# Performance work log

Measured on AMD Instinct MI355X. Metric: run time of the kernel, lower is better.

Reference implementation:

```python
import jax, jax.numpy as jnp
import numpy as np

N = 512          # pedestrians in scene
T = 12           # decode steps
OBS = 8
FEAT = 2
LAT = 32
COND = 64
LSTM_IN = 128
HID = 64         # lstm_hidden_size == context_state_size
CTX = 64
EMB = 32         # Pooling_net spatial embedding dim
MLP_IN = EMB + 2 * CTX   # 160
MLP_MID = 64
BOT = CTX        # bottleneck_dim = h_dim
IN_DEC = COND + LAT + CTX + FEAT  # 162


def setup_inputs() -> dict:
    key = jax.random.key(0)
    ks = jax.random.split(key, 24)
    s = 0.1
    return {
        "last_position": jax.random.normal(ks[0], (N, FEAT), jnp.float32),
        "c": jax.random.normal(ks[1], (N, COND), jnp.float32),
        "z": jax.random.normal(ks[2], (N, LAT), jnp.float32),
        "obs_traj_pos": jax.random.normal(ks[3], (OBS, N, FEAT), jnp.float32),
        "nei_index": jax.random.randint(ks[4], (T, N, N), 0, 2, jnp.int32),
        "nei_num_index": jax.random.randint(ks[5], (N,), 0, N, jnp.int32),
        "h0": jax.random.normal(ks[6], (N, HID), jnp.float32),
        "c0": jax.random.normal(ks[7], (N, HID), jnp.float32),
        "eps": jax.random.normal(ks[8], (T, N, FEAT), jnp.float32),
        "W_in": jax.random.normal(ks[9], (IN_DEC, LSTM_IN), jnp.float32) * s,
        "b_in": jnp.zeros((LSTM_IN,), jnp.float32),
        "W_ih": jax.random.normal(ks[10], (4 * HID, LSTM_IN), jnp.float32) * s,
        "W_hh": jax.random.normal(ks[11], (4 * HID, HID), jnp.float32) * s,
        "b_ih": jnp.zeros((4 * HID,), jnp.float32),
        "b_hh": jnp.zeros((4 * HID,), jnp.float32),
        "W_l2p": jax.random.normal(ks[12], (HID // 2 + CTX, FEAT), jnp.float32) * s,
        "b_l2p": jnp.zeros((FEAT,), jnp.float32),
        "W_sp": jax.random.normal(ks[13], (FEAT, EMB), jnp.float32) * s,
        "b_sp": jnp.zeros((EMB,), jnp.float32),
        "W1": jax.random.normal(ks[14], (MLP_IN, MLP_MID), jnp.float32) * s,
        "b1": jnp.zeros((MLP_MID,), jnp.float32),
        "W2": jax.random.normal(ks[15], (MLP_MID, BOT), jnp.float32) * s,
        "b2": jnp.zeros((BOT,), jnp.float32),
    }


def reference(last_position, c, z, obs_traj_pos, nei_index, nei_num_index,
              h0, c0, eps, W_in, b_in, W_ih, W_hh, b_ih, b_hh,
              W_l2p, b_l2p, W_sp, b_sp, W1, b1, W2, b2):
    sg = jax.lax.stop_gradient
    half = HID // 2
    neg_inf = jnp.float32(-jnp.inf)

    def pooling(mask, lstm_state, pos):
        # mask: [N,N] bool; lstm_state: [N,CTX]; pos: [N,2]
        corr = pos[:, None, :] - pos[None, :, :]           # [N,N,2] pos[i]-pos[j]
        r = corr @ W_sp + b_sp                              # [N,N,EMB]
        hj = jnp.broadcast_to(lstm_state[None, :, :], (N, N, CTX))
        hi = jnp.broadcast_to(lstm_state[:, None, :], (N, N, CTX))
        x = jnp.concatenate([r, hj, hi], axis=-1)           # [N,N,160]
        h1 = jax.nn.relu(x @ W1 + b1)
        h2 = jax.nn.relu(h1 @ W2 + b2)                      # [N,N,BOT]
        Hm = jnp.where(mask[:, :, None], h2, neg_inf)       # scatter of valid rows
        pool = Hm.max(axis=1)                               # max over neighbors j
        return jnp.where(pool == neg_inf, 0.0, pool)

    def lstm_cell(x, h, cs):
        gates = x @ W_ih.T + b_ih + h @ W_hh.T + b_hh
        i, f, g, o = jnp.split(gates, 4, axis=-1)
        c_new = jax.nn.sigmoid(f) * cs + jax.nn.sigmoid(i) * jnp.tanh(g)
        h_new = jax.nn.sigmoid(o) * jnp.tanh(c_new)
        return h_new, c_new

    def step(carry, xs):
        prev_pos, h, cs, ctx, cur_abs = carry
        nei_t, eps_t = xs
        emb = jnp.concatenate([sg(prev_pos), sg(c), sg(z), sg(ctx)], axis=-1)
        x = jax.nn.relu(emb @ W_in + b_in)
        h, cs = lstm_cell(x, h, cs)
        ctx = pooling(nei_t > 0, h, cur_abs)
        mu = jnp.concatenate([h[:, :half], ctx], -1) @ W_l2p + b_l2p
        logvar = jnp.concatenate([h[:, half:], ctx], -1) @ W_l2p + b_l2p
        pos = mu + eps_t * jnp.exp(0.5 * logvar)
        cur_abs = sg(cur_abs + pos)
        return (pos, h, cs, ctx, cur_abs), (pos, mu, logvar)

    ctx0 = jnp.zeros((N, CTX), jnp.float32)
    carry0 = (last_position, h0, c0, ctx0, obs_traj_pos[-1])
    _, (pre_pos, mean, var) = jax.lax.scan(step, carry0, (nei_index, eps))
    return pre_pos, mean, var
```

## Files before the change

kernel.cpp:

```cpp
#include <hip/hip_runtime.h>
#include <math.h>

#define NP 512
#define TT 12

typedef float f32x4 __attribute__((ext_vector_type(4)));
typedef __bf16 bf16x8 __attribute__((ext_vector_type(8)));

#define OFF_CURABS 0
#define OFF_A      2048
#define OFF_B      67584
#define OFF_H      100352
#define OFF_CS     133120
#define OFF_WIHT   165888
#define OFF_WHHT   198656
#define OFF_WC     215040
#define OFF_BASE   215168

__global__ __launch_bounds__(256) void init_k(
    const float* __restrict__ obs, const float* __restrict__ W_ih,
    const float* __restrict__ W_hh, const float* __restrict__ W_sp,
    const float* __restrict__ b_sp, const float* __restrict__ W1,
    const float* __restrict__ b1, float* __restrict__ ws) {
  int tid = blockIdx.x * 256 + threadIdx.x;
  if (tid < 1024) ws[OFF_CURABS + tid] = obs[7 * 1024 + tid];
  if (tid < 32768) {
    int k = tid >> 8, g = tid & 255;
    ws[OFF_WIHT + tid] = W_ih[g * 128 + k];
  }
  if (tid < 16384) {
    int k = tid >> 8, g = tid & 255;
    ws[OFF_WHHT + tid] = W_hh[g * 64 + k];
  }
  if (tid < 128) {
    int d = tid >> 6, m = tid & 63;
    float s = 0.f;
    for (int e = 0; e < 32; ++e) s = fmaf(W_sp[d * 32 + e], W1[e * 64 + m], s);
    ws[OFF_WC + tid] = s;
  }
  if (tid < 64) {
    float s = b1[tid];
    for (int e = 0; e < 32; ++e) s = fmaf(b_sp[e], W1[e * 64 + tid], s);
    ws[OFF_BASE + tid] = s;
  }
}

__global__ __launch_bounds__(256) void step_k(
    const float* __restrict__ lastpos, const float* __restrict__ cc,
    const float* __restrict__ zz, const int* __restrict__ nei,
    const float* __restrict__ h0, const float* __restrict__ c0,
    const float* __restrict__ epsin,
    const float* __restrict__ W_in, const float* __restrict__ b_in,
    const float* __restrict__ b_ih, const float* __restrict__ b_hh,
    const float* __restrict__ Wl2p, const float* __restrict__ bl2p,
    const float* __restrict__ W1, const float* __restrict__ W2,
    const float* __restrict__ b2,
    float* __restrict__ out, float* __restrict__ ws, int s) {
  __shared__ __align__(16) __bf16 h1buf[4][32 * 72];
  __shared__ __align__(16) __bf16 W2T[64 * 72];
  __shared__ float absx[512], absy[512];
  __shared__ int   ml[512];
  __shared__ float wcl[128], bib[64], basev[64];
  __shared__ float red[4][64];
  __shared__ float hloc[64], csloc[64], ctxloc[64], prevp[2];
  __shared__ float emb[162], xpart[2][128], xvec[128], gl[256];

  int t = threadIdx.x;
  int b = blockIdx.x;
  int lane = t & 63, w = t >> 6;
  int quad = lane >> 4, col = lane & 15;

  if (t < 64) {
    if (s == 0) { hloc[t] = h0[b * 64 + t]; csloc[t] = c0[b * 64 + t]; ctxloc[t] = 0.f; }
    else        { hloc[t] = ws[OFF_H + b * 64 + t]; csloc[t] = ws[OFF_CS + b * 64 + t]; }
    basev[t] = ws[OFF_BASE + t];
  } else if (t < 192) {
    wcl[t - 64] = ws[OFF_WC + (t - 64)];
  } else if (s > 0) {
    bib[t - 192] = ws[OFF_B + b * 64 + (t - 192)];
  }
  if (s == 0 && t < 2) prevp[t] = lastpos[b * 2 + t];
  if (s > 0) {
    for (int e = t; e < 4096; e += 256)
      W2T[(e & 63) * 72 + (e >> 6)] = (__bf16)W2[e];
  }
  __syncthreads();

  if (s > 0) {
    int st = s - 1;
    bf16x8 bf00 = *(const bf16x8*)&W2T[(0 * 16 + col) * 72 + 0 * 32 + quad * 8];
    bf16x8 bf01 = *(const bf16x8*)&W2T[(0 * 16 + col) * 72 + 1 * 32 + quad * 8];
    bf16x8 bf10 = *(const bf16x8*)&W2T[(1 * 16 + col) * 72 + 0 * 32 + quad * 8];
    bf16x8 bf11 = *(const bf16x8*)&W2T[(1 * 16 + col) * 72 + 1 * 32 + quad * 8];
    bf16x8 bf20 = *(const bf16x8*)&W2T[(2 * 16 + col) * 72 + 0 * 32 + quad * 8];
    bf16x8 bf21 = *(const bf16x8*)&W2T[(2 * 16 + col) * 72 + 1 * 32 + quad * 8];
    bf16x8 bf30 = *(const bf16x8*)&W2T[(3 * 16 + col) * 72 + 0 * 32 + quad * 8];
    bf16x8 bf31 = *(const bf16x8*)&W2T[(3 * 16 + col) * 72 + 1 * 32 + quad * 8];
    float b2v0 = b2[col], b2v1 = b2[16 + col], b2v2 = b2[32 + col], b2v3 = b2[48 + col];

    int rb = st & 1, wbuf = rb ^ 1;
    const float* curabs  = ws + OFF_CURABS + rb * 1024;
    float*       curabsw = ws + OFF_CURABS + wbuf * 1024;
    const float* Aab = ws + OFF_A + rb * 32768;
    const int* neirow = nei + ((size_t)st * NP + b) * NP;
    {
      const float2* ca = (const float2*)curabs;
      for (int j = t; j < 512; j += 256) {
        float2 p = ca[j];
        absx[j] = p.x; absy[j] = p.y;
        ml[j] = neirow[j];
      }
    }
    __syncthreads();

    float px = absx[b], py = absy[b];
    float wcx = wcl[lane], wcy = wcl[64 + lane];
    float bi  = bib[lane];
    float vmax0 = 0.f, vmax1 = 0.f, vmax2 = 0.f, vmax3 = 0.f;
    __bf16* myh1 = h1buf[w];

    for (int c = 0; c < 4; ++c) {
      int jbase = w * 128 + c * 32;
      #pragma unroll 4
      for (int j = 0; j < 32; ++j) {
        int jg = jbase + j;
        float v = fmaf(px - absx[jg], wcx,
                  fmaf(py - absy[jg], wcy, Aab[jg * 64 + lane] + bi));
        myh1[j * 72 + lane] = (__bf16)fmaxf(v, 0.f);
      }
      #pragma unroll
      for (int js = 0; js < 2; ++js) {
        bf16x8 a0 = *(const bf16x8*)&myh1[(js * 16 + col) * 72 + 0 * 32 + quad * 8];
        bf16x8 a1 = *(const bf16x8*)&myh1[(js * 16 + col) * 72 + 1 * 32 + quad * 8];
        int rowb = jbase + js * 16 + quad * 4;
        bool mk0 = ml[rowb] > 0, mk1 = ml[rowb + 1] > 0,
             mk2 = ml[rowb + 2] > 0, mk3 = ml[rowb + 3] > 0;
        f32x4 acc;
        acc = (f32x4){0.f, 0.f, 0.f, 0.f};
        acc = __builtin_amdgcn_mfma_f32_16x16x32_bf16(a0, bf00, acc, 0, 0, 0);
        acc = __builtin_amdgcn_mfma_f32_16x16x32_bf16(a1, bf01, acc, 0, 0, 0);
        vmax0 = fmaxf(vmax0, mk0 ? acc[0] + b2v0 : 0.f);
        vmax0 = fmaxf(vmax0, mk1 ? acc[1] + b2v0 : 0.f);
        vmax0 = fmaxf(vmax0, mk2 ? acc[2] + b2v0 : 0.f);
        vmax0 = fmaxf(vmax0, mk3 ? acc[3] + b2v0 : 0.f);
        acc = (f32x4){0.f, 0.f, 0.f, 0.f};
        acc = __builtin_amdgcn_mfma_f32_16x16x32_bf16(a0, bf10, acc, 0, 0, 0);
        acc = __builtin_amdgcn_mfma_f32_16x16x32_bf16(a1, bf11, acc, 0, 0, 0);
        vmax1 = fmaxf(vmax1, mk0 ? acc[0] + b2v1 : 0.f);
        vmax1 = fmaxf(vmax1, mk1 ? acc[1] + b2v1 : 0.f);
        vmax1 = fmaxf(vmax1, mk2 ? acc[2] + b2v1 : 0.f);
        vmax1 = fmaxf(vmax1, mk3 ? acc[3] + b2v1 : 0.f);
        acc = (f32x4){0.f, 0.f, 0.f, 0.f};
        acc = __builtin_amdgcn_mfma_f32_16x16x32_bf16(a0, bf20, acc, 0, 0, 0);
        acc = __builtin_amdgcn_mfma_f32_16x16x32_bf16(a1, bf21, acc, 0, 0, 0);
        vmax2 = fmaxf(vmax2, mk0 ? acc[0] + b2v2 : 0.f);
        vmax2 = fmaxf(vmax2, mk1 ? acc[1] + b2v2 : 0.f);
        vmax2 = fmaxf(vmax2, mk2 ? acc[2] + b2v2 : 0.f);
        vmax2 = fmaxf(vmax2, mk3 ? acc[3] + b2v2 : 0.f);
        acc = (f32x4){0.f, 0.f, 0.f, 0.f};
        acc = __builtin_amdgcn_mfma_f32_16x16x32_bf16(a0, bf30, acc, 0, 0, 0);
        acc = __builtin_amdgcn_mfma_f32_16x16x32_bf16(a1, bf31, acc, 0, 0, 0);
        vmax3 = fmaxf(vmax3, mk0 ? acc[0] + b2v3 : 0.f);
        vmax3 = fmaxf(vmax3, mk1 ? acc[1] + b2v3 : 0.f);
        vmax3 = fmaxf(vmax3, mk2 ? acc[2] + b2v3 : 0.f);
        vmax3 = fmaxf(vmax3, mk3 ? acc[3] + b2v3 : 0.f);
      }
    }
    vmax0 = fmaxf(vmax0, __shfl_xor(vmax0, 16));
    vmax0 = fmaxf(vmax0, __shfl_xor(vmax0, 32));
    vmax1 = fmaxf(vmax1, __shfl_xor(vmax1, 16));
    vmax1 = fmaxf(vmax1, __shfl_xor(vmax1, 32));
    vmax2 = fmaxf(vmax2, __shfl_xor(vmax2, 16));
    vmax2 = fmaxf(vmax2, __shfl_xor(vmax2, 32));
    vmax3 = fmaxf(vmax3, __shfl_xor(vmax3, 16));
    vmax3 = fmaxf(vmax3, __shfl_xor(vmax3, 32));
    if (lane < 16) {
      red[w][0 * 16 + lane] = vmax0;
      red[w][1 * 16 + lane] = vmax1;
      red[w][2 * 16 + lane] = vmax2;
      red[w][3 * 16 + lane] = vmax3;
    }
    __syncthreads();
    if (t < 64) {
      float m4 = fmaxf(fmaxf(red[0][t], red[1][t]),
                       fmaxf(red[2][t], red[3][t]));
      ctxloc[t] = m4;
    }
    __syncthreads();
    if (t < 64) {
      int l = t;
      float cl = ctxloc[l];
      float sc0 = cl * Wl2p[(32 + l) * 2 + 0];
      float sc1 = cl * Wl2p[(32 + l) * 2 + 1];
      float m0 = 0.f, m1 = 0.f, v0 = 0.f, v1 = 0.f;
      if (l < 32) {
        float hm = hloc[l];
        m0 = hm * Wl2p[l * 2 + 0]; m1 = hm * Wl2p[l * 2 + 1];
        float hv = hloc[32 + l];
        v0 = hv * Wl2p[l * 2 + 0]; v1 = hv * Wl2p[l * 2 + 1];
      }
      for (int off = 32; off >= 1; off >>= 1) {
        sc0 += __shfl_down(sc0, off);
        sc1 += __shfl_down(sc1, off);
        m0  += __shfl_down(m0,  off);
        m1  += __shfl_down(m1,  off);
        v0  += __shfl_down(v0,  off);
        v1  += __shfl_down(v1,  off);
      }
      if (l == 0) {
        float mu0 = m0 + sc0 + bl2p[0], mu1 = m1 + sc1 + bl2p[1];
        float lv0 = v0 + sc0 + bl2p[0], lv1 = v1 + sc1 + bl2p[1];
        float e0 = epsin[st * 1024 + b * 2 + 0];
        float e1 = epsin[st * 1024 + b * 2 + 1];
        float p0 = mu0 + e0 * expf(0.5f * lv0);
        float p1 = mu1 + e1 * expf(0.5f * lv1);
        out[st * 1024 + b * 2 + 0] = p0;
        out[st * 1024 + b * 2 + 1] = p1;
        out[12288 + st * 1024 + b * 2 + 0] = mu0;
        out[12288 + st * 1024 + b * 2 + 1] = mu1;
        out[24576 + st * 1024 + b * 2 + 0] = lv0;
        out[24576 + st * 1024 + b * 2 + 1] = lv1;
        curabsw[b * 2 + 0] = px + p0;
        curabsw[b * 2 + 1] = py + p1;
        prevp[0] = p0;
        prevp[1] = p1;
      }
    }
    __syncthreads();
  }

  if (s < TT) {
    if (t < 162) {
      float v;
      if (t < 2)       v = prevp[t];
      else if (t < 66) v = cc[b * 64 + (t - 2)];
      else if (t < 98) v = zz[b * 32 + (t - 66)];
      else             v = ctxloc[t - 98];
      emb[t] = v;
    }
    __syncthreads();
    {
      int k = t & 127, p = t >> 7;
      float a0 = 0.f, a1 = 0.f;
      int d = p;
      for (; d + 2 < 162; d += 4) {
        a0 = fmaf(emb[d],     W_in[d * 128 + k],       a0);
        a1 = fmaf(emb[d + 2], W_in[(d + 2) * 128 + k], a1);
      }
      if (d < 162) a0 = fmaf(emb[d], W_in[d * 128 + k], a0);
      xpart[p][k] = a0 + a1;
    }
    __syncthreads();
    if (t < 128) xvec[t] = fmaxf(xpart[0][t] + xpart[1][t] + b_in[t], 0.f);
    __syncthreads();
    {
      int g = t;
      const float* wiht = ws + OFF_WIHT;
      const float* whht = ws + OFF_WHHT;
      float s0 = 0.f, s1 = 0.f, s2 = 0.f, s3 = 0.f;
      for (int kk = 0; kk < 128; kk += 4) {
        s0 = fmaf(xvec[kk],     wiht[kk * 256 + g],       s0);
        s1 = fmaf(xvec[kk + 1], wiht[(kk + 1) * 256 + g], s1);
        s2 = fmaf(xvec[kk + 2], wiht[(kk + 2) * 256 + g], s2);
        s3 = fmaf(xvec[kk + 3], wiht[(kk + 3) * 256 + g], s3);
      }
      for (int kk = 0; kk < 64; kk += 4) {
        s0 = fmaf(hloc[kk],     whht[kk * 256 + g],       s0);
        s1 = fmaf(hloc[kk + 1], whht[(kk + 1) * 256 + g], s1);
        s2 = fmaf(hloc[kk + 2], whht[(kk + 2) * 256 + g], s2);
        s3 = fmaf(hloc[kk + 3], whht[(kk + 3) * 256 + g], s3);
      }
      gl[g] = b_ih[g] + b_hh[g] + ((s0 + s1) + (s2 + s3));
    }
    __syncthreads();
    if (t < 64) {
      float ig = gl[t], fg = gl[64 + t], gg = gl[128 + t], og = gl[192 + t];
      float is = 1.f / (1.f + expf(-ig));
      float fs = 1.f / (1.f + expf(-fg));
      float os = 1.f / (1.f + expf(-og));
      float cn = fs * csloc[t] + is * tanhf(gg);
      float hv = os * tanhf(cn);
      hloc[t] = hv;
      ws[OFF_CS + b * 64 + t] = cn;
      ws[OFF_H + b * 64 + t] = hv;
    }
    __syncthreads();
    if (t < 128) {
      int which = t >> 6, m = t & 63;
      const float* wb = W1 + (32 + which * 64) * 64 + m;
      float s0 = 0.f, s1 = 0.f, s2 = 0.f, s3 = 0.f;
      for (int k = 0; k < 64; k += 4) {
        s0 = fmaf(hloc[k],     wb[k * 64],       s0);
        s1 = fmaf(hloc[k + 1], wb[(k + 1) * 64], s1);
        s2 = fmaf(hloc[k + 2], wb[(k + 2) * 64], s2);
        s3 = fmaf(hloc[k + 3], wb[(k + 3) * 64], s3);
      }
      float sv = (s0 + s1) + (s2 + s3);
      if (which == 0) ws[OFF_A + (s & 1) * 32768 + b * 64 + m] = sv + basev[m];
      else            ws[OFF_B + b * 64 + m] = sv;
    }
  }
}

extern "C" void kernel_launch(void* const* d_in, const int* in_sizes, int n_in,
                              void* d_out, int out_size, void* d_ws, size_t ws_size,
                              hipStream_t stream) {
  const float* lastpos = (const float*)d_in[0];
  const float* cc      = (const float*)d_in[1];
  const float* zz      = (const float*)d_in[2];
  const float* obs     = (const float*)d_in[3];
  const int*   nei     = (const int*)d_in[4];
  const float* h0      = (const float*)d_in[6];
  const float* c0      = (const float*)d_in[7];
  const float* eps     = (const float*)d_in[8];
  const float* W_in    = (const float*)d_in[9];
  const float* b_in    = (const float*)d_in[10];
  const float* W_ih    = (const float*)d_in[11];
  const float* W_hh    = (const float*)d_in[12];
  const float* b_ih    = (const float*)d_in[13];
  const float* b_hh    = (const float*)d_in[14];
  const float* W_l2p   = (const float*)d_in[15];
  const float* b_l2p   = (const float*)d_in[16];
  const float* W_sp    = (const float*)d_in[17];
  const float* b_sp    = (const float*)d_in[18];
  const float* W1      = (const float*)d_in[19];
  const float* b1      = (const float*)d_in[20];
  const float* W2      = (const float*)d_in[21];
  const float* b2      = (const float*)d_in[22];
  float* out = (float*)d_out;
  float* ws  = (float*)d_ws;

  hipLaunchKernelGGL(init_k, dim3(128), dim3(256), 0, stream,
                     obs, W_ih, W_hh, W_sp, b_sp, W1, b1, ws);
  for (int s = 0; s <= TT; ++s) {
    hipLaunchKernelGGL(step_k, dim3(NP), dim3(256), 0, stream,
                       lastpos, cc, zz, nei, h0, c0, eps,
                       W_in, b_in, b_ih, b_hh, W_l2p, b_l2p,
                       W1, W2, b2, out, ws, s);
  }
}
```

Baseline: 394.5 us.

## Fold position terms into per-node Q/P vectors and feed MFMA directly from registers

Rewrites the first pooling-MLP layer algebraically. Each node's relative-position term is split into a per-neighbour part Q_j (A_j minus Wc·pos_j) and a per-target part P_i (B_i plus Wc·pos_i), so the hidden activation becomes relu(Q_j + P_i). The MFMA A operands are then built in registers from vectorized global loads of Q, which removes the per-element LDS staging buffer, the absx/absy arrays and one block barrier. The bias add and relu of the second layer move after the max reduction, with -1e30 used as the masked identity. This adds reliance on floating-point reassociation and on how masked rows are handled when no neighbour is present.

```diff
diff --git a/kernel.cpp b/kernel.cpp
--- a/kernel.cpp
+++ b/kernel.cpp
@@ -8,14 +8,14 @@
 typedef __bf16 bf16x8 __attribute__((ext_vector_type(8)));
 
 #define OFF_CURABS 0
-#define OFF_A      2048
-#define OFF_B      67584
-#define OFF_H      100352
-#define OFF_CS     133120
-#define OFF_WIHT   165888
-#define OFF_WHHT   198656
-#define OFF_WC     215040
-#define OFF_BASE   215168
+#define OFF_Q      2048
+#define OFF_P      67584
+#define OFF_WIHT   100352
+#define OFF_WHHT   133120
+#define OFF_WC     149504
+#define OFF_BASE   149632
+#define OFF_H      149696
+#define OFF_CS     182464
 
 __global__ __launch_bounds__(256) void init_k(
     const float* __restrict__ obs, const float* __restrict__ W_ih,
@@ -49,20 +49,18 @@
     const float* __restrict__ lastpos, const float* __restrict__ cc,
     const float* __restrict__ zz, const int* __restrict__ nei,
     const float* __restrict__ h0, const float* __restrict__ c0,
-    const float* __restrict__ epsin,
+    const float* __restrict__ obs, const float* __restrict__ epsin,
     const float* __restrict__ W_in, const float* __restrict__ b_in,
     const float* __restrict__ b_ih, const float* __restrict__ b_hh,
     const float* __restrict__ Wl2p, const float* __restrict__ bl2p,
     const float* __restrict__ W1, const float* __restrict__ W2,
     const float* __restrict__ b2,
     float* __restrict__ out, float* __restrict__ ws, int s) {
-  __shared__ __align__(16) __bf16 h1buf[4][32 * 72];
   __shared__ __align__(16) __bf16 W2T[64 * 72];
-  __shared__ float absx[512], absy[512];
   __shared__ int   ml[512];
-  __shared__ float wcl[128], bib[64], basev[64];
+  __shared__ float wcl[128], basev[64];
   __shared__ float red[4][64];
-  __shared__ float hloc[64], csloc[64], ctxloc[64], prevp[2];
+  __shared__ float hloc[64], csloc[64], ctxloc[64], prevp[2], pxy[2];
   __shared__ float emb[162], xpart[2][128], xvec[128], gl[256];
 
   int t = threadIdx.x;
@@ -76,18 +74,22 @@
     basev[t] = ws[OFF_BASE + t];
   } else if (t < 192) {
     wcl[t - 64] = ws[OFF_WC + (t - 64)];
-  } else if (s > 0) {
-    bib[t - 192] = ws[OFF_B + b * 64 + (t - 192)];
-  }
-  if (s == 0 && t < 2) prevp[t] = lastpos[b * 2 + t];
+  }
+  if (s == 0 && t < 2) {
+    prevp[t] = lastpos[b * 2 + t];
+    pxy[t]   = obs[7 * 1024 + b * 2 + t];
+  }
   if (s > 0) {
     for (int e = t; e < 4096; e += 256)
       W2T[(e & 63) * 72 + (e >> 6)] = (__bf16)W2[e];
+    const int* neirow = nei + ((size_t)(s - 1) * NP + b) * NP;
+    for (int j = t; j < 512; j += 256) ml[j] = neirow[j];
   }
   __syncthreads();
 
   if (s > 0) {
     int st = s - 1;
+    const float* Qb = ws + OFF_Q + (st & 1) * 32768;
     bf16x8 bf00 = *(const bf16x8*)&W2T[(0 * 16 + col) * 72 + 0 * 32 + quad * 8];
     bf16x8 bf01 = *(const bf16x8*)&W2T[(0 * 16 + col) * 72 + 1 * 32 + quad * 8];
     bf16x8 bf10 = *(const bf16x8*)&W2T[(1 * 16 + col) * 72 + 0 * 32 + quad * 8];
@@ -96,75 +98,61 @@
     bf16x8 bf21 = *(const bf16x8*)&W2T[(2 * 16 + col) * 72 + 1 * 32 + quad * 8];
     bf16x8 bf30 = *(const bf16x8*)&W2T[(3 * 16 + col) * 72 + 0 * 32 + quad * 8];
     bf16x8 bf31 = *(const bf16x8*)&W2T[(3 * 16 + col) * 72 + 1 * 32 + quad * 8];
-    float b2v0 = b2[col], b2v1 = b2[16 + col], b2v2 = b2[32 + col], b2v3 = b2[48 + col];
-
-    int rb = st & 1, wbuf = rb ^ 1;
-    const float* curabs  = ws + OFF_CURABS + rb * 1024;
-    float*       curabsw = ws + OFF_CURABS + wbuf * 1024;
-    const float* Aab = ws + OFF_A + rb * 32768;
-    const int* neirow = nei + ((size_t)st * NP + b) * NP;
-    {
-      const float2* ca = (const float2*)curabs;
-      for (int j = t; j < 512; j += 256) {
-        float2 p = ca[j];
-        absx[j] = p.x; absy[j] = p.y;
-        ml[j] = neirow[j];
-      }
-    }
-    __syncthreads();
-
-    float px = absx[b], py = absy[b];
-    float wcx = wcl[lane], wcy = wcl[64 + lane];
-    float bi  = bib[lane];
-    float vmax0 = 0.f, vmax1 = 0.f, vmax2 = 0.f, vmax3 = 0.f;
-    __bf16* myh1 = h1buf[w];
-
-    for (int c = 0; c < 4; ++c) {
-      int jbase = w * 128 + c * 32;
-      #pragma unroll 4
-      for (int j = 0; j < 32; ++j) {
-        int jg = jbase + j;
-        float v = fmaf(px - absx[jg], wcx,
-                  fmaf(py - absy[jg], wcy, Aab[jg * 64 + lane] + bi));
-        myh1[j * 72 + lane] = (__bf16)fmaxf(v, 0.f);
-      }
+    float pl0[8], pl1[8];
+    #pragma unroll
+    for (int e = 0; e < 8; ++e) {
+      pl0[e] = ws[OFF_P + b * 64 + quad * 8 + e];
+      pl1[e] = ws[OFF_P + b * 64 + 32 + quad * 8 + e];
+    }
+    float vmax0 = -1e30f, vmax1 = -1e30f, vmax2 = -1e30f, vmax3 = -1e30f;
+
+    for (int c = 0; c < 8; ++c) {
+      int j0 = w * 128 + c * 16;
+      int jr = (j0 + col) * 64 + quad * 8;
+      f32x4 qa = *(const f32x4*)&Qb[jr];
+      f32x4 qb = *(const f32x4*)&Qb[jr + 4];
+      f32x4 qc = *(const f32x4*)&Qb[jr + 32];
+      f32x4 qd = *(const f32x4*)&Qb[jr + 36];
+      bf16x8 a0, a1;
       #pragma unroll
-      for (int js = 0; js < 2; ++js) {
-        bf16x8 a0 = *(const bf16x8*)&myh1[(js * 16 + col) * 72 + 0 * 32 + quad * 8];
-        bf16x8 a1 = *(const bf16x8*)&myh1[(js * 16 + col) * 72 + 1 * 32 + quad * 8];
-        int rowb = jbase + js * 16 + quad * 4;
-        bool mk0 = ml[rowb] > 0, mk1 = ml[rowb + 1] > 0,
-             mk2 = ml[rowb + 2] > 0, mk3 = ml[rowb + 3] > 0;
-        f32x4 acc;
-        acc = (f32x4){0.f, 0.f, 0.f, 0.f};
-        acc = __builtin_amdgcn_mfma_f32_16x16x32_bf16(a0, bf00, acc, 0, 0, 0);
-        acc = __builtin_amdgcn_mfma_f32_16x16x32_bf16(a1, bf01, acc, 0, 0, 0);
-        vmax0 = fmaxf(vmax0, mk0 ? acc[0] + b2v0 : 0.f);
-        vmax0 = fmaxf(vmax0, mk1 ? acc[1] + b2v0 : 0.f);
-        vmax0 = fmaxf(vmax0, mk2 ? acc[2] + b2v0 : 0.f);
-        vmax0 = fmaxf(vmax0, mk3 ? acc[3] + b2v0 : 0.f);
-        acc = (f32x4){0.f, 0.f, 0.f, 0.f};
-        acc = __builtin_amdgcn_mfma_f32_16x16x32_bf16(a0, bf10, acc, 0, 0, 0);
-        acc = __builtin_amdgcn_mfma_f32_16x16x32_bf16(a1, bf11, acc, 0, 0, 0);
-        vmax1 = fmaxf(vmax1, mk0 ? acc[0] + b2v1 : 0.f);
-        vmax1 = fmaxf(vmax1, mk1 ? acc[1] + b2v1 : 0.f);
-        vmax1 = fmaxf(vmax1, mk2 ? acc[2] + b2v1 : 0.f);
-        vmax1 = fmaxf(vmax1, mk3 ? acc[3] + b2v1 : 0.f);
-        acc = (f32x4){0.f, 0.f, 0.f, 0.f};
-        acc = __builtin_amdgcn_mfma_f32_16x16x32_bf16(a0, bf20, acc, 0, 0, 0);
-        acc = __builtin_amdgcn_mfma_f32_16x16x32_bf16(a1, bf21, acc, 0, 0, 0);
-        vmax2 = fmaxf(vmax2, mk0 ? acc[0] + b2v2 : 0.f);
-        vmax2 = fmaxf(vmax2, mk1 ? acc[1] + b2v2 : 0.f);
-        vmax2 = fmaxf(vmax2, mk2 ? acc[2] + b2v2 : 0.f);
-        vmax2 = fmaxf(vmax2, mk3 ? acc[3] + b2v2 : 0.f);
-        acc = (f32x4){0.f, 0.f, 0.f, 0.f};
-        acc = __builtin_amdgcn_mfma_f32_16x16x32_bf16(a0, bf30, acc, 0, 0, 0);
-        acc = __builtin_amdgcn_mfma_f32_16x16x32_bf16(a1, bf31, acc, 0, 0, 0);
-        vmax3 = fmaxf(vmax3, mk0 ? acc[0] + b2v3 : 0.f);
-        vmax3 = fmaxf(vmax3, mk1 ? acc[1] + b2v3 : 0.f);
-        vmax3 = fmaxf(vmax3, mk2 ? acc[2] + b2v3 : 0.f);
-        vmax3 = fmaxf(vmax3, mk3 ? acc[3] + b2v3 : 0.f);
-      }
+      for (int e = 0; e < 4; ++e) {
+        a0[e]     = (__bf16)fmaxf(qa[e] + pl0[e],     0.f);
+        a0[e + 4] = (__bf16)fmaxf(qb[e] + pl0[e + 4], 0.f);
+        a1[e]     = (__bf16)fmaxf(qc[e] + pl1[e],     0.f);
+        a1[e + 4] = (__bf16)fmaxf(qd[e] + pl1[e + 4], 0.f);
+      }
+      int mrow = j0 + quad * 4;
+      bool mk0 = ml[mrow] > 0, mk1 = ml[mrow + 1] > 0,
+           mk2 = ml[mrow + 2] > 0, mk3 = ml[mrow + 3] > 0;
+      f32x4 acc;
+      acc = (f32x4){0.f, 0.f, 0.f, 0.f};
+      acc = __builtin_amdgcn_mfma_f32_16x16x32_bf16(a0, bf00, acc, 0, 0, 0);
+      acc = __builtin_amdgcn_mfma_f32_16x16x32_bf16(a1, bf01, acc, 0, 0, 0);
+      vmax0 = fmaxf(vmax0, mk0 ? acc[0] : -1e30f);
+      vmax0 = fmaxf(vmax0, mk1 ? acc[1] : -1e30f);
+      vmax0 = fmaxf(vmax0, mk2 ? acc[2] : -1e30f);
+      vmax0 = fmaxf(vmax0, mk3 ? acc[3] : -1e30f);
+      acc = (f32x4){0.f, 0.f, 0.f, 0.f};
+      acc = __builtin_amdgcn_mfma_f32_16x16x32_bf16(a0, bf10, acc, 0, 0, 0);
+      acc = __builtin_amdgcn_mfma_f32_16x16x32_bf16(a1, bf11, acc, 0, 0, 0);
+      vmax1 = fmaxf(vmax1, mk0 ? acc[0] : -1e30f);
+      vmax1 = fmaxf(vmax1, mk1 ? acc[1] : -1e30f);
+      vmax1 = fmaxf(vmax1, mk2 ? acc[2] : -1e30f);
+      vmax1 = fmaxf(vmax1, mk3 ? acc[3] : -1e30f);
+      acc = (f32x4){0.f, 0.f, 0.f, 0.f};
+      acc = __builtin_amdgcn_mfma_f32_16x16x32_bf16(a0, bf20, acc, 0, 0, 0);
+      acc = __builtin_amdgcn_mfma_f32_16x16x32_bf16(a1, bf21, acc, 0, 0, 0);
+      vmax2 = fmaxf(vmax2, mk0 ? acc[0] : -1e30f);
+      vmax2 = fmaxf(vmax2, mk1 ? acc[1] : -1e30f);
+      vmax2 = fmaxf(vmax2, mk2 ? acc[2] : -1e30f);
+      vmax2 = fmaxf(vmax2, mk3 ? acc[3] : -1e30f);
+      acc = (f32x4){0.f, 0.f, 0.f, 0.f};
+      acc = __builtin_amdgcn_mfma_f32_16x16x32_bf16(a0, bf30, acc, 0, 0, 0);
+      acc = __builtin_amdgcn_mfma_f32_16x16x32_bf16(a1, bf31, acc, 0, 0, 0);
+      vmax3 = fmaxf(vmax3, mk0 ? acc[0] : -1e30f);
+      vmax3 = fmaxf(vmax3, mk1 ? acc[1] : -1e30f);
+      vmax3 = fmaxf(vmax3, mk2 ? acc[2] : -1e30f);
+      vmax3 = fmaxf(vmax3, mk3 ? acc[3] : -1e30f);
     }
     vmax0 = fmaxf(vmax0, __shfl_xor(vmax0, 16));
     vmax0 = fmaxf(vmax0, __shfl_xor(vmax0, 32));
@@ -184,7 +172,7 @@
     if (t < 64) {
       float m4 = fmaxf(fmaxf(red[0][t], red[1][t]),
                        fmaxf(red[2][t], red[3][t]));
-      ctxloc[t] = m4;
+      ctxloc[t] = fmaxf(m4 + b2[t], 0.f);
     }
     __syncthreads();
     if (t < 64) {
@@ -220,10 +208,13 @@
         out[12288 + st * 1024 + b * 2 + 1] = mu1;
         out[24576 + st * 1024 + b * 2 + 0] = lv0;
         out[24576 + st * 1024 + b * 2 + 1] = lv1;
-        curabsw[b * 2 + 0] = px + p0;
-        curabsw[b * 2 + 1] = py + p1;
-        prevp[0] = p0;
-        prevp[1] = p1;
+        float px = ws[OFF_CURABS + (st & 1) * 1024 + b * 2 + 0];
+        float py = ws[OFF_CURABS + (st & 1) * 1024 + b * 2 + 1];
+        float nx = px + p0, ny = py + p1;
+        ws[OFF_CURABS + ((st & 1) ^ 1) * 1024 + b * 2 + 0] = nx;
+        ws[OFF_CURABS + ((st & 1) ^ 1) * 1024 + b * 2 + 1] = ny;
+        pxy[0] = nx; pxy[1] = ny;
+        prevp[0] = p0; prevp[1] = p1;
       }
     }
     __syncthreads();
@@ -296,8 +287,12 @@
         s3 = fmaf(hloc[k + 3], wb[(k + 3) * 64], s3);
       }
       float sv = (s0 + s1) + (s2 + s3);
-      if (which == 0) ws[OFF_A + (s & 1) * 32768 + b * 64 + m] = sv + basev[m];
-      else            ws[OFF_B + b * 64 + m] = sv;
+      float cx = pxy[0], cy = pxy[1];
+      if (which == 0)
+        ws[OFF_Q + (s & 1) * 32768 + b * 64 + m] =
+            sv + basev[m] - cx * wcl[m] - cy * wcl[64 + m];
+      else
+        ws[OFF_P + b * 64 + m] = sv + cx * wcl[m] + cy * wcl[64 + m];
     }
   }
 }
@@ -334,7 +329,7 @@
                      obs, W_ih, W_hh, W_sp, b_sp, W1, b1, ws);
   for (int s = 0; s <= TT; ++s) {
     hipLaunchKernelGGL(step_k, dim3(NP), dim3(256), 0, stream,
-                       lastpos, cc, zz, nei, h0, c0, eps,
+                       lastpos, cc, zz, nei, h0, c0, obs, eps,
                        W_in, b_in, b_ih, b_hh, W_l2p, b_l2p,
                        W1, W2, b2, out, ws, s);
   }
```

After: 369.4 us. 1.07x faster.
